# Performance work log

Hardware: AMD Instinct MI355X
Metric: run time of the kernel (lower is better)

## Reference

```python
import jax, jax.numpy as jnp
import numpy as np

STATE_DIM = 512
HYPER_EMBED = 1024
MIX_EMBED = 256
N_AGENTS = 32
B = 8192


def setup_inputs() -> dict:
    key = jax.random.key(0)
    ks = jax.random.split(key, 16)
    s = lambda k, shape, fan_in: jax.random.normal(k, shape, jnp.float32) / np.sqrt(fan_in)
    return {
        "agent_qs": jax.random.normal(ks[0], (B, N_AGENTS), jnp.float32),
        "states": jax.random.normal(ks[1], (B, STATE_DIM), jnp.float32),
        # hyper_w_1: Linear(S,H) -> ReLU -> Linear(H, E*A)
        "hw1_w1": s(ks[2], (STATE_DIM, HYPER_EMBED), STATE_DIM),
        "hw1_b1": jnp.zeros((HYPER_EMBED,), jnp.float32),
        "hw1_w2": s(ks[3], (HYPER_EMBED, MIX_EMBED * N_AGENTS), HYPER_EMBED),
        "hw1_b2": jnp.zeros((MIX_EMBED * N_AGENTS,), jnp.float32),
        # hyper_b_1: Linear(S, E)
        "hb1_w": s(ks[4], (STATE_DIM, MIX_EMBED), STATE_DIM),
        "hb1_b": jnp.zeros((MIX_EMBED,), jnp.float32),
        # hyper_w_final: Linear(S,H) -> ReLU -> Linear(H, E)
        "hwf_w1": s(ks[5], (STATE_DIM, HYPER_EMBED), STATE_DIM),
        "hwf_b1": jnp.zeros((HYPER_EMBED,), jnp.float32),
        "hwf_w2": s(ks[6], (HYPER_EMBED, MIX_EMBED), HYPER_EMBED),
        "hwf_b2": jnp.zeros((MIX_EMBED,), jnp.float32),
        # V: Linear(S,E) -> ReLU -> Linear(E, 1)
        "v_w1": s(ks[7], (STATE_DIM, MIX_EMBED), STATE_DIM),
        "v_b1": jnp.zeros((MIX_EMBED,), jnp.float32),
        "v_w2": s(ks[8], (MIX_EMBED, 1), MIX_EMBED),
        "v_b2": jnp.zeros((1,), jnp.float32),
    }


def reference(agent_qs, states, hw1_w1, hw1_b1, hw1_w2, hw1_b2, hb1_w, hb1_b,
              hwf_w1, hwf_b1, hwf_w2, hwf_b2, v_w1, v_b1, v_w2, v_b2):
    st = states.reshape(-1, STATE_DIM)                       # [B, S]
    # hypernetwork-generated first-layer weights and bias
    h1 = jax.nn.relu(st @ hw1_w1 + hw1_b1)                   # [B, H]
    w1 = jnp.abs(h1 @ hw1_w2 + hw1_b2).reshape(-1, N_AGENTS, MIX_EMBED)  # [B, A, E]
    b1 = (st @ hb1_w + hb1_b)[:, None, :]                    # [B, 1, E]
    q = agent_qs.reshape(-1, 1, N_AGENTS)                    # [B, 1, A]
    hidden = jax.nn.elu(jnp.einsum('bia,bae->bie', q, w1) + b1)  # [B, 1, E]
    # hypernetwork-generated final-layer weights
    hf = jax.nn.relu(st @ hwf_w1 + hwf_b1)                   # [B, H]
    w_final = jnp.abs(hf @ hwf_w2 + hwf_b2)[:, :, None]      # [B, E, 1]
    # state-dependent value bias
    v = (jax.nn.relu(st @ v_w1 + v_b1) @ v_w2 + v_b2)[:, :, None]  # [B, 1, 1]
    q_tot = jnp.einsum('bie,bej->bij', hidden, w_final) + v  # [B, 1, 1]
    return q_tot
```

## Files before the change

kernel.cpp:

```cpp
#include <hip/hip_runtime.h>
#include <hip/hip_bf16.h>

#define B_SZ 8192
#define S_DIM 512
#define H_DIM 1024
#define E_DIM 256
#define A_DIM 32

typedef __attribute__((ext_vector_type(4))) float f32x4;
typedef __attribute__((ext_vector_type(8))) __bf16 bf16x8;
typedef __attribute__((ext_vector_type(4))) int i32x4;
typedef __attribute__((ext_vector_type(8))) int i32x8;

using as1_void = __attribute__((address_space(1))) void;
using as3_void = __attribute__((address_space(3))) void;

__device__ __forceinline__ unsigned short f2bfu(float f) {
  unsigned u = __builtin_bit_cast(unsigned, f);
  unsigned r = (u + 0x7FFFu + ((u >> 16) & 1u)) >> 16;
  return (unsigned short)r;
}
__device__ __forceinline__ float bf2f(unsigned short x) {
  unsigned u = ((unsigned)x) << 16;
  return __builtin_bit_cast(float, u);
}
__device__ __forceinline__ unsigned char f2fp8(float f) {
  return (unsigned char)(__builtin_amdgcn_cvt_pk_fp8_f32(f, f, 0, false) & 0xFF);
}

__device__ __forceinline__ float row16_sum(float s) {
  float t;
  t = __builtin_bit_cast(float, __builtin_amdgcn_update_dpp(
          0, __builtin_bit_cast(int, s), 0xB1, 0xF, 0xF, true));
  s += t;
  t = __builtin_bit_cast(float, __builtin_amdgcn_update_dpp(
          0, __builtin_bit_cast(int, s), 0x4E, 0xF, 0xF, true));
  s += t;
  t = __builtin_bit_cast(float, __builtin_amdgcn_update_dpp(
          0, __builtin_bit_cast(int, s), 0x141, 0xF, 0xF, true));
  s += t;
  t = __builtin_bit_cast(float, __builtin_amdgcn_update_dpp(
          0, __builtin_bit_cast(int, s), 0x140, 0xF, 0xF, true));
  s += t;
  return s;
}

#define PREPA_BLOCKS 5418
__global__ void prepA_kernel(const float* __restrict__ states, const float* __restrict__ hw1_w1,
                             const float* __restrict__ hwf_w1, const float* __restrict__ hb1_w,
                             const float* __restrict__ v_w1, const float* __restrict__ hw1_b1,
                             const float* __restrict__ hwf_b1, const float* __restrict__ hb1_b,
                             const float* __restrict__ v_b1, const float* __restrict__ hw1_b2,
                             unsigned short* __restrict__ st_bf, unsigned short* __restrict__ wcat,
                             float* __restrict__ bcatp, float* __restrict__ bias_p) {
  __shared__ float t[32][33];
  const int tid = threadIdx.x;
  int b = blockIdx.x;
  if (b < 4096) {
    int idx = b * 1024 + tid * 4;
    const float4 v = *(const float4*)(states + idx);
    ushort4 o;
    o.x = f2bfu(v.x); o.y = f2bfu(v.y); o.z = f2bfu(v.z); o.w = f2bfu(v.w);
    *(ushort4*)(st_bf + idx) = o;
    return;
  }
  b -= 4096;
  if (b >= 1280) {
    b -= 1280;
    if (b < 10) {
      int i = b * 256 + tid;
      if (i < 2560) {
        float v;
        if (i < 1024) v = hw1_b1[i];
        else if (i < 2048) v = hwf_b1[i - 1024];
        else if (i < 2304) v = hb1_b[i - 2048];
        else v = v_b1[i - 2304];
        bcatp[i] = v;
      }
    } else {
      int n = (b - 10) * 256 + tid;
      bias_p[n] = hw1_b2[((n & 31) << 8) + (n >> 5)];
    }
    return;
  }
  const float* src;
  unsigned short* dst;
  int C, tile;
  if (b < 512) { src = hw1_w1; dst = wcat; C = 1024; tile = b; }
  else if (b < 1024) { src = hwf_w1; dst = wcat + (size_t)1024 * 512; C = 1024; tile = b - 512; }
  else if (b < 1152) { src = hb1_w; dst = wcat + (size_t)2048 * 512; C = 256; tile = b - 1024; }
  else { src = v_w1; dst = wcat + (size_t)2304 * 512; C = 256; tile = b - 1152; }
  const int R = 512;
  const int tpc = C >> 5;
  const int c0 = (tile % tpc) * 32, r0 = (tile / tpc) * 32;
  const int tx = tid & 31, ty = tid >> 5;
#pragma unroll
  for (int i = 0; i < 4; ++i) {
    int r = r0 + ty + i * 8;
    t[ty + i * 8][tx] = src[(size_t)r * C + c0 + tx];
  }
  __syncthreads();
#pragma unroll
  for (int i = 0; i < 4; ++i) {
    int c = c0 + ty + i * 8;
    dst[(size_t)c * R + r0 + tx] = f2bfu(t[tx][ty + i * 8]);
  }
}

#define FATB_BLOCKS 9728
__global__ __launch_bounds__(256, 2) void fatB_kernel(
    const unsigned short* __restrict__ st_bf, const unsigned short* __restrict__ wcat,
    const float* __restrict__ bcatp, unsigned short* __restrict__ ocat,
    unsigned char* __restrict__ a8, const float* __restrict__ hw1_w2,
    const float* __restrict__ hwf_w2, unsigned char* __restrict__ w8T,
    unsigned short* __restrict__ wf2T) {
  __shared__ __align__(16) unsigned char smem[32768];
  const int tid = threadIdx.x;
  int b = blockIdx.x;
  if (b < 1280) {
    unsigned short* As = (unsigned short*)smem;
    unsigned short* Bs = (unsigned short*)(smem + 16384);
    const int w = tid >> 6, l = tid & 63;
    const int wr = w >> 1, wc = w & 1;
    const int col0 = (b % 20) * 128, row0 = (b / 20) * 128;
    const int K = 512, N = 2560, Astr = 512;
    f32x4 acc[4][4] = {};
    for (int k0 = 0; k0 < K; k0 += 64) {
      __syncthreads();
#pragma unroll
      for (int i = 0; i < 4; ++i) {
        int cbase = i * 256 + w * 64;
        int c = cbase + l;
        int r = c >> 3, kc = c & 7;
        const unsigned short* src = st_bf + (size_t)(row0 + r) * Astr + (k0 + kc * 8);
        __builtin_amdgcn_global_load_lds((const as1_void*)src, (as3_void*)&As[cbase * 8], 16, 0, 0);
      }
#pragma unroll
      for (int i = 0; i < 4; ++i) {
        int cbase = i * 256 + w * 64;
        int c = cbase + l;
        int r = c >> 3, kc = c & 7;
        const unsigned short* src = wcat + (size_t)(col0 + r) * K + (k0 + kc * 8);
        __builtin_amdgcn_global_load_lds((const as1_void*)src, (as3_void*)&Bs[cbase * 8], 16, 0, 0);
      }
      __syncthreads();
#pragma unroll
      for (int kk = 0; kk < 2; ++kk) {
        bf16x8 af[4], bfr[4];
#pragma unroll
        for (int i = 0; i < 4; ++i)
          af[i] = *(const bf16x8*)&As[(wr * 64 + i * 16 + (l & 15)) * 64 + kk * 32 + (l >> 4) * 8];
#pragma unroll
        for (int j = 0; j < 4; ++j)
          bfr[j] = *(const bf16x8*)&Bs[(wc * 64 + j * 16 + (l & 15)) * 64 + kk * 32 + (l >> 4) * 8];
#pragma unroll
        for (int i = 0; i < 4; ++i)
#pragma unroll
          for (int j = 0; j < 4; ++j)
            acc[i][j] = __builtin_amdgcn_mfma_f32_16x16x32_bf16(af[i], bfr[j], acc[i][j], 0, 0, 0);
      }
    }
#pragma unroll
    for (int i = 0; i < 4; ++i)
#pragma unroll
      for (int j = 0; j < 4; ++j)
#pragma unroll
        for (int t = 0; t < 4; ++t) {
          int r = row0 + wr * 64 + i * 16 + (l >> 4) * 4 + t;
          int c = col0 + wc * 64 + j * 16 + (l & 15);
          float v = acc[i][j][t] + bcatp[c];
          if (!(c >= 2048 && c < 2304)) v = fmaxf(v, 0.0f);
          if (c < 1024)
            a8[(size_t)r * 1024 + c] = f2fp8(v);
          else
            ocat[(size_t)r * N + c] = f2bfu(v);
        }
    return;
  }
  b -= 1280;
  {
    float(*t)[33] = (float(*)[33])smem;
    const float* src;
    int C, tile;
    bool perm;
    if (b < 8192) { src = hw1_w2; C = 8192; tile = b; perm = true; }
    else { src = hwf_w2; C = 256; tile = b - 8192; perm = false; }
    const int R = 1024;
    const int tpc = C >> 5;
    const int c0 = (tile % tpc) * 32, r0 = (tile / tpc) * 32;
    const int tx = tid & 31, ty = tid >> 5;
#pragma unroll
    for (int i = 0; i < 4; ++i) {
      int r = r0 + ty + i * 8;
      t[ty + i * 8][tx] = src[(size_t)r * C + c0 + tx];
    }
    __syncthreads();
#pragma unroll
    for (int i = 0; i < 4; ++i) {
      int c = c0 + ty + i * 8;
      if (perm) {
        size_t co = (size_t)(((c & 255) << 5) + (c >> 8));
        w8T[co * 1024 + r0 + tx] = f2fp8(t[tx][ty + i * 8]);
      } else {
        wf2T[(size_t)c * R + r0 + tx] = f2bfu(t[tx][ty + i * 8]);
      }
    }
  }
}

__global__ void wf_gemm_kernel(const unsigned short* __restrict__ A, int Astr,
                               const unsigned short* __restrict__ BT,
                               const float* __restrict__ bias, unsigned short* __restrict__ Cp,
                               int M, int N, int K) {
  __shared__ unsigned short As[128 * 64];
  __shared__ unsigned short Bs[128 * 64];
  const int tid = threadIdx.x;
  const int w = tid >> 6, l = tid & 63;
  const int wr = w >> 1, wc = w & 1;
  const int row0 = blockIdx.y * 128, col0 = blockIdx.x * 128;
  f32x4 acc[4][4] = {};
  for (int k0 = 0; k0 < K; k0 += 64) {
    __syncthreads();
#pragma unroll
    for (int i = 0; i < 4; ++i) {
      int cbase = i * 256 + w * 64;
      int c = cbase + l;
      int r = c >> 3, kc = c & 7;
      const unsigned short* src = A + (size_t)(row0 + r) * Astr + (k0 + kc * 8);
      __builtin_amdgcn_global_load_lds((const as1_void*)src, (as3_void*)&As[cbase * 8], 16, 0, 0);
    }
#pragma unroll
    for (int i = 0; i < 4; ++i) {
      int cbase = i * 256 + w * 64;
      int c = cbase + l;
      int r = c >> 3, kc = c & 7;
      const unsigned short* src = BT + (size_t)(col0 + r) * K + (k0 + kc * 8);
      __builtin_amdgcn_global_load_lds((const as1_void*)src, (as3_void*)&Bs[cbase * 8], 16, 0, 0);
    }
    __syncthreads();
#pragma unroll
    for (int kk = 0; kk < 2; ++kk) {
      bf16x8 af[4], bfr[4];
#pragma unroll
      for (int i = 0; i < 4; ++i)
        af[i] = *(const bf16x8*)&As[(wr * 64 + i * 16 + (l & 15)) * 64 + kk * 32 + (l >> 4) * 8];
#pragma unroll
      for (int j = 0; j < 4; ++j)
        bfr[j] = *(const bf16x8*)&Bs[(wc * 64 + j * 16 + (l & 15)) * 64 + kk * 32 + (l >> 4) * 8];
#pragma unroll
      for (int i = 0; i < 4; ++i)
#pragma unroll
        for (int j = 0; j < 4; ++j)
          acc[i][j] = __builtin_amdgcn_mfma_f32_16x16x32_bf16(af[i], bfr[j], acc[i][j], 0, 0, 0);
    }
  }
#pragma unroll
  for (int i = 0; i < 4; ++i)
#pragma unroll
    for (int j = 0; j < 4; ++j)
#pragma unroll
      for (int t = 0; t < 4; ++t) {
        int r = row0 + wr * 64 + i * 16 + (l >> 4) * 4 + t;
        int c = col0 + wc * 64 + j * 16 + (l & 15);
        Cp[(size_t)r * N + c] = f2bfu(fabsf(acc[i][j][t] + bias[c]));
      }
}

__global__ __launch_bounds__(256, 2) void gemm128_f8(
    const unsigned char* __restrict__ A, const unsigned char* __restrict__ BT,
    const float* __restrict__ bias, const float* __restrict__ qs,
    float* __restrict__ hid, int M, int N, int K) {
  __shared__ __align__(16) unsigned char As[128 * 128];
  __shared__ __align__(16) unsigned char Bs[128 * 128];
  const int tid = threadIdx.x;
  const int w = tid >> 6, l = tid & 63;
  const int wr = w >> 1, wc = w & 1;
  const int row0 = blockIdx.y * 128, col0 = blockIdx.x * 128;
  f32x4 acc[4][4] = {};
  for (int k0 = 0; k0 < K; k0 += 128) {
    __syncthreads();
#pragma unroll
    for (int i = 0; i < 4; ++i) {
      int cbase = i * 256 + w * 64;
      int c = cbase + l;
      int r = c >> 3, kc = c & 7;
      const unsigned char* src = A + (size_t)(row0 + r) * K + (k0 + ((kc ^ (r & 7)) << 4));
      __builtin_amdgcn_global_load_lds((const as1_void*)src, (as3_void*)&As[cbase * 16], 16, 0, 0);
    }
#pragma unroll
    for (int i = 0; i < 4; ++i) {
      int cbase = i * 256 + w * 64;
      int c = cbase + l;
      int r = c >> 3, kc = c & 7;
      const unsigned char* src = BT + (size_t)(col0 + r) * K + (k0 + ((kc ^ (r & 7)) << 4));
      __builtin_amdgcn_global_load_lds((const as1_void*)src, (as3_void*)&Bs[cbase * 16], 16, 0, 0);
    }
    __syncthreads();
    i32x8 af[4], bfr[4];
#pragma unroll
    for (int i = 0; i < 4; ++i) {
      const int r = wr * 64 + i * 16 + (l & 15);
      const int kc = (l >> 4) * 2;
      i32x4 lo = *(const i32x4*)&As[r * 128 + ((kc ^ (r & 7)) << 4)];
      i32x4 hi = *(const i32x4*)&As[r * 128 + (((kc + 1) ^ (r & 7)) << 4)];
      af[i] = __builtin_shufflevector(lo, hi, 0, 1, 2, 3, 4, 5, 6, 7);
    }
#pragma unroll
    for (int j = 0; j < 4; ++j) {
      const int r = wc * 64 + j * 16 + (l & 15);
      const int kc = (l >> 4) * 2;
      i32x4 lo = *(const i32x4*)&Bs[r * 128 + ((kc ^ (r & 7)) << 4)];
      i32x4 hi = *(const i32x4*)&Bs[r * 128 + (((kc + 1) ^ (r & 7)) << 4)];
      bfr[j] = __builtin_shufflevector(lo, hi, 0, 1, 2, 3, 4, 5, 6, 7);
    }
    __builtin_amdgcn_s_setprio(1);
#pragma unroll
    for (int i = 0; i < 4; ++i)
#pragma unroll
      for (int j = 0; j < 4; ++j)
        acc[i][j] = __builtin_amdgcn_mfma_scale_f32_16x16x128_f8f6f4(
            af[i], bfr[j], acc[i][j], 0, 0, 0, 127, 0, 127);
    __builtin_amdgcn_s_setprio(0);
  }

  float qv[4][4][2];
  float bp[4];
#pragma unroll
  for (int i = 0; i < 4; ++i)
#pragma unroll
    for (int tt = 0; tt < 4; ++tt) {
      const int r = row0 + wr * 64 + i * 16 + (l >> 4) * 4 + tt;
      qv[i][tt][0] = qs[(size_t)r * A_DIM + (l & 15)];
      qv[i][tt][1] = qs[(size_t)r * A_DIM + 16 + (l & 15)];
    }
#pragma unroll
  for (int j = 0; j < 4; ++j)
    bp[j] = bias[col0 + wc * 64 + j * 16 + (l & 15)];
#pragma unroll
  for (int i = 0; i < 4; ++i)
#pragma unroll
    for (int e2 = 0; e2 < 2; ++e2) {
      const int e = (col0 >> 5) + wc * 2 + e2;
#pragma unroll
      for (int tt = 0; tt < 4; ++tt) {
        const int r = row0 + wr * 64 + i * 16 + (l >> 4) * 4 + tt;
        float s = fmaf(qv[i][tt][0], fabsf(acc[i][e2 * 2][tt] + bp[e2 * 2]), 0.0f);
        s = fmaf(qv[i][tt][1], fabsf(acc[i][e2 * 2 + 1][tt] + bp[e2 * 2 + 1]), s);
        s = row16_sum(s);
        if ((l & 15) == 0) hid[(size_t)r * E_DIM + e] = s;
      }
    }
}

__global__ void final2_kernel(const float* __restrict__ hid, const unsigned short* __restrict__ b1p,
                              const unsigned short* __restrict__ vhp, int ostr,
                              const unsigned short* __restrict__ wf,
                              const float* __restrict__ vw2, const float* __restrict__ vb2,
                              float* __restrict__ out) {
  const int tid = threadIdx.x;
  const int b = blockIdx.x;
  float h = hid[(size_t)b * E_DIM + tid] + bf2f(b1p[(size_t)b * ostr + tid]);
  float hidden = h > 0.0f ? h : (expf(h) - 1.0f);
  float s = hidden * bf2f(wf[(size_t)b * E_DIM + tid]) +
            bf2f(vhp[(size_t)b * ostr + tid]) * vw2[tid];
  __shared__ float red[4];
#pragma unroll
  for (int o = 32; o > 0; o >>= 1) s += __shfl_down(s, o, 64);
  if ((tid & 63) == 0) red[tid >> 6] = s;
  __syncthreads();
  if (tid == 0) out[b] = red[0] + red[1] + red[2] + red[3] + vb2[0];
}

extern "C" void kernel_launch(void* const* d_in, const int* in_sizes, int n_in,
                              void* d_out, int out_size, void* d_ws, size_t ws_size,
                              hipStream_t stream) {
  const float* agent_qs = (const float*)d_in[0];
  const float* states = (const float*)d_in[1];
  const float* hw1_w1 = (const float*)d_in[2];
  const float* hw1_b1 = (const float*)d_in[3];
  const float* hw1_w2 = (const float*)d_in[4];
  const float* hw1_b2 = (const float*)d_in[5];
  const float* hb1_w = (const float*)d_in[6];
  const float* hb1_b = (const float*)d_in[7];
  const float* hwf_w1 = (const float*)d_in[8];
  const float* hwf_b1 = (const float*)d_in[9];
  const float* hwf_w2 = (const float*)d_in[10];
  const float* hwf_b2 = (const float*)d_in[11];
  const float* v_w1 = (const float*)d_in[12];
  const float* v_b1 = (const float*)d_in[13];
  const float* v_w2 = (const float*)d_in[14];
  const float* v_b2 = (const float*)d_in[15];
  float* out = (float*)d_out;

  size_t off = 0;
  char* ws = (char*)d_ws;
  auto carve = [&](size_t bytes) -> void* {
    void* p = ws + off;
    off = (off + bytes + 255) & ~(size_t)255;
    return p;
  };
  const int NCAT = 2560;
  unsigned short* st_bf = (unsigned short*)carve((size_t)B_SZ * S_DIM * 2);
  unsigned short* wcat = (unsigned short*)carve((size_t)NCAT * S_DIM * 2);
  unsigned char* w8T = (unsigned char*)carve((size_t)8192 * H_DIM);
  unsigned short* wf2T = (unsigned short*)carve((size_t)E_DIM * H_DIM * 2);
  float* bcatp = (float*)carve((size_t)NCAT * 4);
  float* bias_p = (float*)carve((size_t)8192 * 4);
  unsigned short* ocat = (unsigned short*)carve((size_t)B_SZ * NCAT * 2);
  unsigned char* a8 = (unsigned char*)carve((size_t)B_SZ * H_DIM);
  unsigned short* wfb = (unsigned short*)carve((size_t)B_SZ * E_DIM * 2);
  float* hid = (float*)carve((size_t)B_SZ * E_DIM * 4);

  prepA_kernel<<<PREPA_BLOCKS, 256, 0, stream>>>(
      states, hw1_w1, hwf_w1, hb1_w, v_w1, hw1_b1, hwf_b1, hb1_b, v_b1, hw1_b2,
      st_bf, wcat, bcatp, bias_p);

  fatB_kernel<<<FATB_BLOCKS, 256, 0, stream>>>(
      st_bf, wcat, bcatp, ocat, a8, hw1_w2, hwf_w2, w8T, wf2T);

  wf_gemm_kernel<<<dim3(E_DIM / 128, B_SZ / 128), 256, 0, stream>>>(
      ocat + 1024, NCAT, wf2T, hwf_b2, wfb, B_SZ, E_DIM, H_DIM);

  gemm128_f8<<<dim3(8192 / 128, B_SZ / 128), 256, 0, stream>>>(
      a8, w8T, bias_p, agent_qs, hid, B_SZ, 8192, H_DIM);

  final2_kernel<<<B_SZ, 256, 0, stream>>>(hid, ocat + 2048, ocat + 2304, NCAT, wfb, v_w2, v_b2, out);
}
```

Baseline: 150.3 us.

## Load FP8 GEMM fragments directly from global memory, bypassing LDS staging

The FP8 GEMM kernel no longer stages A and B tiles through shared memory with global_load_lds and barriers. Each lane now reads its MFMA fragments straight from global memory using precomputed row pointers, and the k-loop is unrolled by two. This removes the LDS round trip and both __syncthreads per iteration. In exchange, each element is fetched by both waves that share a tile row or column, which leans on L1/L2 caching, and there is no explicit prefetch or pipelining.

```diff
diff --git a/kernel.cpp b/kernel.cpp
--- a/kernel.cpp
+++ b/kernel.cpp
@@ -270,47 +270,33 @@
     const unsigned char* __restrict__ A, const unsigned char* __restrict__ BT,
     const float* __restrict__ bias, const float* __restrict__ qs,
     float* __restrict__ hid, int M, int N, int K) {
-  __shared__ __align__(16) unsigned char As[128 * 128];
-  __shared__ __align__(16) unsigned char Bs[128 * 128];
   const int tid = threadIdx.x;
   const int w = tid >> 6, l = tid & 63;
   const int wr = w >> 1, wc = w & 1;
   const int row0 = blockIdx.y * 128, col0 = blockIdx.x * 128;
+  const int kl = (l >> 4) * 32;
+  const unsigned char* ar[4];
+  const unsigned char* br[4];
+#pragma unroll
+  for (int i = 0; i < 4; ++i)
+    ar[i] = A + (size_t)(row0 + wr * 64 + i * 16 + (l & 15)) * K + kl;
+#pragma unroll
+  for (int j = 0; j < 4; ++j)
+    br[j] = BT + (size_t)(col0 + wc * 64 + j * 16 + (l & 15)) * K + kl;
   f32x4 acc[4][4] = {};
+#pragma unroll 2
   for (int k0 = 0; k0 < K; k0 += 128) {
-    __syncthreads();
+    i32x8 af[4], bfr[4];
 #pragma unroll
     for (int i = 0; i < 4; ++i) {
-      int cbase = i * 256 + w * 64;
-      int c = cbase + l;
-      int r = c >> 3, kc = c & 7;
-      const unsigned char* src = A + (size_t)(row0 + r) * K + (k0 + ((kc ^ (r & 7)) << 4));
-      __builtin_amdgcn_global_load_lds((const as1_void*)src, (as3_void*)&As[cbase * 16], 16, 0, 0);
-    }
-#pragma unroll
-    for (int i = 0; i < 4; ++i) {
-      int cbase = i * 256 + w * 64;
-      int c = cbase + l;
-      int r = c >> 3, kc = c & 7;
-      const unsigned char* src = BT + (size_t)(col0 + r) * K + (k0 + ((kc ^ (r & 7)) << 4));
-      __builtin_amdgcn_global_load_lds((const as1_void*)src, (as3_void*)&Bs[cbase * 16], 16, 0, 0);
-    }
-    __syncthreads();
-    i32x8 af[4], bfr[4];
-#pragma unroll
-    for (int i = 0; i < 4; ++i) {
-      const int r = wr * 64 + i * 16 + (l & 15);
-      const int kc = (l >> 4) * 2;
-      i32x4 lo = *(const i32x4*)&As[r * 128 + ((kc ^ (r & 7)) << 4)];
-      i32x4 hi = *(const i32x4*)&As[r * 128 + (((kc + 1) ^ (r & 7)) << 4)];
+      i32x4 lo = *(const i32x4*)(ar[i] + k0);
+      i32x4 hi = *(const i32x4*)(ar[i] + k0 + 16);
       af[i] = __builtin_shufflevector(lo, hi, 0, 1, 2, 3, 4, 5, 6, 7);
     }
 #pragma unroll
     for (int j = 0; j < 4; ++j) {
-      const int r = wc * 64 + j * 16 + (l & 15);
-      const int kc = (l >> 4) * 2;
-      i32x4 lo = *(const i32x4*)&Bs[r * 128 + ((kc ^ (r & 7)) << 4)];
-      i32x4 hi = *(const i32x4*)&Bs[r * 128 + (((kc + 1) ^ (r & 7)) << 4)];
+      i32x4 lo = *(const i32x4*)(br[j] + k0);
+      i32x4 hi = *(const i32x4*)(br[j] + k0 + 16);
       bfr[j] = __builtin_shufflevector(lo, hi, 0, 1, 2, 3, 4, 5, 6, 7);
     }
     __builtin_amdgcn_s_setprio(1);
```

Measured after the change: 313.7 us. 2.09x slower.

## Double-buffer LDS tiles in fp8 GEMM to overlap global loads with MFMA

Applied to the files above, without the earlier changes.

Splits the A and B shared-memory tiles of the fp8 hypernetwork GEMM into two buffers. The loads for tile k+1 are issued directly to LDS before the MFMA work on tile k, so each K step costs one barrier instead of two. The aim is to hide global-load latency behind compute. This doubles LDS use to 64KB per block, which may cut occupancy under launch_bounds(256,2). It also depends on a manual vmcnt wait for correctness, since LDS reads of the current buffer must finish before the next iteration overwrites it.

```diff
diff --git a/kernel.cpp b/kernel.cpp
--- a/kernel.cpp
+++ b/kernel.cpp
@@ -14,6 +14,8 @@
 
 using as1_void = __attribute__((address_space(1))) void;
 using as3_void = __attribute__((address_space(3))) void;
+
+#define WAITV0 asm volatile("s_waitcnt vmcnt(0)" ::: "memory")
 
 __device__ __forceinline__ unsigned short f2bfu(float f) {
   unsigned u = __builtin_bit_cast(unsigned, f);
@@ -270,22 +272,22 @@
     const unsigned char* __restrict__ A, const unsigned char* __restrict__ BT,
     const float* __restrict__ bias, const float* __restrict__ qs,
     float* __restrict__ hid, int M, int N, int K) {
-  __shared__ __align__(16) unsigned char As[128 * 128];
-  __shared__ __align__(16) unsigned char Bs[128 * 128];
+  __shared__ __align__(16) unsigned char As[2][128 * 128];
+  __shared__ __align__(16) unsigned char Bs[2][128 * 128];
   const int tid = threadIdx.x;
   const int w = tid >> 6, l = tid & 63;
   const int wr = w >> 1, wc = w & 1;
   const int row0 = blockIdx.y * 128, col0 = blockIdx.x * 128;
-  f32x4 acc[4][4] = {};
-  for (int k0 = 0; k0 < K; k0 += 128) {
-    __syncthreads();
+  const int NT = K >> 7;
+
+  auto stage = [&](int buf, int k0) {
 #pragma unroll
     for (int i = 0; i < 4; ++i) {
       int cbase = i * 256 + w * 64;
       int c = cbase + l;
       int r = c >> 3, kc = c & 7;
       const unsigned char* src = A + (size_t)(row0 + r) * K + (k0 + ((kc ^ (r & 7)) << 4));
-      __builtin_amdgcn_global_load_lds((const as1_void*)src, (as3_void*)&As[cbase * 16], 16, 0, 0);
+      __builtin_amdgcn_global_load_lds((const as1_void*)src, (as3_void*)&As[buf][cbase * 16], 16, 0, 0);
     }
 #pragma unroll
     for (int i = 0; i < 4; ++i) {
@@ -293,24 +295,33 @@
       int c = cbase + l;
       int r = c >> 3, kc = c & 7;
       const unsigned char* src = BT + (size_t)(col0 + r) * K + (k0 + ((kc ^ (r & 7)) << 4));
-      __builtin_amdgcn_global_load_lds((const as1_void*)src, (as3_void*)&Bs[cbase * 16], 16, 0, 0);
-    }
-    __syncthreads();
+      __builtin_amdgcn_global_load_lds((const as1_void*)src, (as3_void*)&Bs[buf][cbase * 16], 16, 0, 0);
+    }
+  };
+
+  f32x4 acc[4][4] = {};
+  stage(0, 0);
+  WAITV0;
+  __builtin_amdgcn_s_barrier();
+
+  for (int t = 0; t < NT; ++t) {
+    const int buf = t & 1;
+    if (t + 1 < NT) stage(buf ^ 1, (t + 1) << 7);
     i32x8 af[4], bfr[4];
 #pragma unroll
     for (int i = 0; i < 4; ++i) {
       const int r = wr * 64 + i * 16 + (l & 15);
       const int kc = (l >> 4) * 2;
-      i32x4 lo = *(const i32x4*)&As[r * 128 + ((kc ^ (r & 7)) << 4)];
-      i32x4 hi = *(const i32x4*)&As[r * 128 + (((kc + 1) ^ (r & 7)) << 4)];
+      i32x4 lo = *(const i32x4*)&As[buf][r * 128 + ((kc ^ (r & 7)) << 4)];
+      i32x4 hi = *(const i32x4*)&As[buf][r * 128 + (((kc + 1) ^ (r & 7)) << 4)];
       af[i] = __builtin_shufflevector(lo, hi, 0, 1, 2, 3, 4, 5, 6, 7);
     }
 #pragma unroll
     for (int j = 0; j < 4; ++j) {
       const int r = wc * 64 + j * 16 + (l & 15);
       const int kc = (l >> 4) * 2;
-      i32x4 lo = *(const i32x4*)&Bs[r * 128 + ((kc ^ (r & 7)) << 4)];
-      i32x4 hi = *(const i32x4*)&Bs[r * 128 + (((kc + 1) ^ (r & 7)) << 4)];
+      i32x4 lo = *(const i32x4*)&Bs[buf][r * 128 + ((kc ^ (r & 7)) << 4)];
+      i32x4 hi = *(const i32x4*)&Bs[buf][r * 128 + (((kc + 1) ^ (r & 7)) << 4)];
       bfr[j] = __builtin_shufflevector(lo, hi, 0, 1, 2, 3, 4, 5, 6, 7);
     }
     __builtin_amdgcn_s_setprio(1);
@@ -321,6 +332,10 @@
         acc[i][j] = __builtin_amdgcn_mfma_scale_f32_16x16x128_f8f6f4(
             af[i], bfr[j], acc[i][j], 0, 0, 0, 127, 0, 127);
     __builtin_amdgcn_s_setprio(0);
+    if (t + 1 < NT) {
+      WAITV0;
+      __builtin_amdgcn_s_barrier();
+    }
   }
 
   float qv[4][4][2];
```

New measurement: 170.7 us. 13.6% more time.

## Fuse final mixing epilogue into fp8 GEMM with atomic accumulation

Applied to the files above, without the earlier changes.

Removes the final2 kernel and the fp32 hid intermediate. The ELU, b1 add and w_final dot product are now computed in the gemm128_f8 epilogue and accumulated into the output with atomicAdd. A small vterm kernel runs first to initialise the output with the value-head term. This saves writing and re-reading an 8 MB buffer and one launch, but adds 64 atomics per output row and an ordering dependency between vterm and the GEMM.

```diff
diff --git a/kernel.cpp b/kernel.cpp
--- a/kernel.cpp
+++ b/kernel.cpp
@@ -11,6 +11,7 @@
 typedef __attribute__((ext_vector_type(8))) __bf16 bf16x8;
 typedef __attribute__((ext_vector_type(4))) int i32x4;
 typedef __attribute__((ext_vector_type(8))) int i32x8;
+typedef __attribute__((ext_vector_type(8))) short short8;
 
 using as1_void = __attribute__((address_space(1))) void;
 using as3_void = __attribute__((address_space(3))) void;
@@ -266,10 +267,27 @@
       }
 }
 
+__global__ void vterm_kernel(const unsigned short* __restrict__ vh, int ostr,
+                             const float* __restrict__ vw2, const float* __restrict__ vb2,
+                             float* __restrict__ out) {
+  const int b = blockIdx.x * 256 + threadIdx.x;
+  const unsigned short* row = vh + (size_t)b * ostr;
+  float s = 0.0f;
+#pragma unroll 4
+  for (int e0 = 0; e0 < E_DIM; e0 += 8) {
+    short8 v = *(const short8*)(row + e0);
+#pragma unroll
+    for (int j = 0; j < 8; ++j)
+      s = fmaf(bf2f((unsigned short)v[j]), vw2[e0 + j], s);
+  }
+  out[b] = s + vb2[0];
+}
+
 __global__ __launch_bounds__(256, 2) void gemm128_f8(
     const unsigned char* __restrict__ A, const unsigned char* __restrict__ BT,
     const float* __restrict__ bias, const float* __restrict__ qs,
-    float* __restrict__ hid, int M, int N, int K) {
+    const unsigned short* __restrict__ b1p, int ostr, const unsigned short* __restrict__ wfb,
+    float* __restrict__ out, int M, int N, int K) {
   __shared__ __align__(16) unsigned char As[128 * 128];
   __shared__ __align__(16) unsigned char Bs[128 * 128];
   const int tid = threadIdx.x;
@@ -336,39 +354,31 @@
 #pragma unroll
   for (int j = 0; j < 4; ++j)
     bp[j] = bias[col0 + wc * 64 + j * 16 + (l & 15)];
+  const int ebase = (col0 >> 5) + wc * 2;
 #pragma unroll
   for (int i = 0; i < 4; ++i)
 #pragma unroll
-    for (int e2 = 0; e2 < 2; ++e2) {
-      const int e = (col0 >> 5) + wc * 2 + e2;
-#pragma unroll
-      for (int tt = 0; tt < 4; ++tt) {
-        const int r = row0 + wr * 64 + i * 16 + (l >> 4) * 4 + tt;
+    for (int tt = 0; tt < 4; ++tt) {
+      const int r = row0 + wr * 64 + i * 16 + (l >> 4) * 4 + tt;
+      float se[2];
+#pragma unroll
+      for (int e2 = 0; e2 < 2; ++e2) {
         float s = fmaf(qv[i][tt][0], fabsf(acc[i][e2 * 2][tt] + bp[e2 * 2]), 0.0f);
         s = fmaf(qv[i][tt][1], fabsf(acc[i][e2 * 2 + 1][tt] + bp[e2 * 2 + 1]), s);
-        s = row16_sum(s);
-        if ((l & 15) == 0) hid[(size_t)r * E_DIM + e] = s;
-      }
-    }
-}
-
-__global__ void final2_kernel(const float* __restrict__ hid, const unsigned short* __restrict__ b1p,
-                              const unsigned short* __restrict__ vhp, int ostr,
-                              const unsigned short* __restrict__ wf,
-                              const float* __restrict__ vw2, const float* __restrict__ vb2,
-                              float* __restrict__ out) {
-  const int tid = threadIdx.x;
-  const int b = blockIdx.x;
-  float h = hid[(size_t)b * E_DIM + tid] + bf2f(b1p[(size_t)b * ostr + tid]);
-  float hidden = h > 0.0f ? h : (expf(h) - 1.0f);
-  float s = hidden * bf2f(wf[(size_t)b * E_DIM + tid]) +
-            bf2f(vhp[(size_t)b * ostr + tid]) * vw2[tid];
-  __shared__ float red[4];
-#pragma unroll
-  for (int o = 32; o > 0; o >>= 1) s += __shfl_down(s, o, 64);
-  if ((tid & 63) == 0) red[tid >> 6] = s;
-  __syncthreads();
-  if (tid == 0) out[b] = red[0] + red[1] + red[2] + red[3] + vb2[0];
+        se[e2] = row16_sum(s);
+      }
+      if ((l & 15) == 0) {
+        float t = 0.0f;
+#pragma unroll
+        for (int e2 = 0; e2 < 2; ++e2) {
+          const int e = ebase + e2;
+          float h = se[e2] + bf2f(b1p[(size_t)r * ostr + e]);
+          float hidden = h > 0.0f ? h : (expf(h) - 1.0f);
+          t = fmaf(hidden, bf2f(wfb[(size_t)r * E_DIM + e]), t);
+        }
+        atomicAdd(&out[r], t);
+      }
+    }
 }
 
 extern "C" void kernel_launch(void* const* d_in, const int* in_sizes, int n_in,
@@ -409,7 +419,6 @@
   unsigned short* ocat = (unsigned short*)carve((size_t)B_SZ * NCAT * 2);
   unsigned char* a8 = (unsigned char*)carve((size_t)B_SZ * H_DIM);
   unsigned short* wfb = (unsigned short*)carve((size_t)B_SZ * E_DIM * 2);
-  float* hid = (float*)carve((size_t)B_SZ * E_DIM * 4);
 
   prepA_kernel<<<PREPA_BLOCKS, 256, 0, stream>>>(
       states, hw1_w1, hwf_w1, hb1_w, v_w1, hw1_b1, hwf_b1, hb1_b, v_b1, hw1_b2,
@@ -421,8 +430,8 @@
   wf_gemm_kernel<<<dim3(E_DIM / 128, B_SZ / 128), 256, 0, stream>>>(
       ocat + 1024, NCAT, wf2T, hwf_b2, wfb, B_SZ, E_DIM, H_DIM);
 
+  vterm_kernel<<<B_SZ / 256, 256, 0, stream>>>(ocat + 2304, NCAT, v_w2, v_b2, out);
+
   gemm128_f8<<<dim3(8192 / 128, B_SZ / 128), 256, 0, stream>>>(
-      a8, w8T, bias_p, agent_qs, hid, B_SZ, 8192, H_DIM);
-
-  final2_kernel<<<B_SZ, 256, 0, stream>>>(hid, ocat + 2048, ocat + 2304, NCAT, wfb, v_w2, v_b2, out);
-}
+      a8, w8T, bias_p, agent_qs, ocat + 2048, NCAT, wfb, out, B_SZ, 8192, H_DIM);
+}
```

Measured after the change: 247.1 us. 64.4% more time.
